# Kernel optimization log

Measured on AMD Instinct MI355X. Metric: run time of the kernel, lower is better.

## Reference

```python
import jax, jax.numpy as jnp
import numpy as np
from jax.ops import segment_sum, segment_max

N, E, F, H, G, P, C = 50000, 600000, 128, 128, 64, 32, 10
HEADS = 3
BN_EPS = 1e-5
COS_EPS = 1e-8


def setup_inputs() -> dict:
    key = jax.random.key(0)
    ks = jax.random.split(key, 32)
    rn = lambda k, shape, s: jax.random.normal(k, shape, jnp.float32) * s
    inp = {
        "x": jax.random.normal(ks[0], (N, F), jnp.float32),
        "edge_index": jax.random.randint(ks[1], (2, E), 0, N, jnp.int32),
        "batch": jnp.sort(jax.random.randint(ks[2], (N,), 0, G, jnp.int32)),
        # GCNConv
        "W1": rn(ks[3], (F, H), F ** -0.5), "b1": jnp.zeros((H,), jnp.float32),
        # SAGEConv (lin_l on aggregated neighbors, lin_r on root)
        "Wl": rn(ks[4], (H, H), H ** -0.5), "Wr": rn(ks[5], (H, H), H ** -0.5),
        "bs": jnp.zeros((H,), jnp.float32),
        # GATConv, heads=3, concat=False
        "Wg": rn(ks[6], (H, HEADS * H), H ** -0.5),
        "a_src": rn(ks[7], (HEADS, H), H ** -0.5),
        "a_dst": rn(ks[8], (HEADS, H), H ** -0.5),
        "bg": jnp.zeros((H,), jnp.float32),
        # prototype head / classifier / decoder
        "protos": jax.random.normal(ks[9], (P, H), jnp.float32),
        "Wc": rn(ks[10], (H, C), H ** -0.5), "bc": jnp.zeros((C,), jnp.float32),
        "Wd1": rn(ks[11], (H, 2 * H), H ** -0.5), "bd1": jnp.zeros((2 * H,), jnp.float32),
        "Wd2": rn(ks[12], (2 * H, F), (2 * H) ** -0.5), "bd2": jnp.zeros((F,), jnp.float32),
    }
    # BatchNorm (eval mode): gamma, beta, running mean/var for bn1..bn3
    for i in range(3):
        k0, k1, k2 = jax.random.split(ks[13 + i], 3)
        inp[f"g{i+1}"] = 1.0 + rn(k0, (H,), 0.05)
        inp[f"be{i+1}"] = rn(k1, (H,), 0.05)
        inp[f"m{i+1}"] = rn(k2, (H,), 0.1)
        inp[f"v{i+1}"] = jnp.ones((H,), jnp.float32)
    return inp


def _bn(x, g, b, m, v):
    return (x - m) * jax.lax.rsqrt(v + BN_EPS) * g + b


def _forward(x, edge_index, batch,
             W1, b1, g1, be1, m1, v1,
             Wl, Wr, bs, g2, be2, m2, v2,
             Wg, a_src, a_dst, bg, g3, be3, m3, v3,
             protos, Wc, bc, Wd1, bd1, Wd2, bd2):
    src, dst = edge_index[0], edge_index[1]
    ones_e = jnp.ones((src.shape[0],), x.dtype)

    # --- GCNConv: symmetric norm with self-loops ---
    h = x @ W1                                        # [N, H]
    deg = segment_sum(ones_e, dst, num_segments=N) + 1.0
    dinv = jax.lax.rsqrt(deg)
    coef = dinv[src] * dinv[dst]                      # [E]
    h1 = segment_sum(h[src] * coef[:, None], dst, num_segments=N)
    h1 = h1 + h * (dinv * dinv)[:, None] + b1         # self-loop term + bias
    h1 = jax.nn.elu(_bn(h1, g1, be1, m1, v1))         # dropout = identity (eval)

    # --- SAGEConv: mean aggregation (no self-loops) ---
    cnt = segment_sum(ones_e, dst, num_segments=N)
    mean_nb = segment_sum(h1[src], dst, num_segments=N) / jnp.maximum(cnt, 1.0)[:, None]
    h2 = mean_nb @ Wl + h1 @ Wr + bs
    h2 = jax.nn.elu(_bn(h2, g2, be2, m2, v2))

    # --- GATConv: heads=3, concat=False (mean), with self-loops ---
    hg = (h2 @ Wg).reshape(N, HEADS, H)               # [N, 3, H]
    al_src = jnp.einsum('nhf,hf->nh', hg, a_src)      # [N, 3]
    al_dst = jnp.einsum('nhf,hf->nh', hg, a_dst)
    loop = jnp.arange(N, dtype=src.dtype)
    s2 = jnp.concatenate([src, loop])
    d2 = jnp.concatenate([dst, loop])
    e = jax.nn.leaky_relu(al_src[s2] + al_dst[d2], 0.2)   # [E+N, 3]
    emax = segment_max(e, d2, num_segments=N)             # every node has a self-loop
    ex = jnp.exp(e - emax[d2])
    den = segment_sum(ex, d2, num_segments=N)
    alpha = ex / den[d2]                                  # [E+N, 3]
    h3 = segment_sum(hg[s2] * alpha[:, :, None], d2, num_segments=N)
    h3 = h3.mean(axis=1) + bg                             # concat=False -> head mean
    h3 = jax.nn.elu(_bn(h3, g3, be3, m3, v3))

    # --- global mean pool over graphs ---
    gcnt = segment_sum(jnp.ones((N,), x.dtype), batch, num_segments=G)
    pooled = segment_sum(h3, batch, num_segments=G) / jnp.maximum(gcnt, 1.0)[:, None]

    # --- prototype head: cosine sim -> softmax -> mix ---
    xn = pooled / jnp.maximum(jnp.linalg.norm(pooled, axis=-1, keepdims=True), COS_EPS)
    pn = protos / jnp.maximum(jnp.linalg.norm(protos, axis=-1, keepdims=True), COS_EPS)
    sims = xn @ pn.T                                      # [G, P]
    assignments = jax.nn.softmax(sims, axis=-1)
    proto_emb = assignments @ protos                      # [G, H]
    logits = proto_emb @ Wc + bc                          # [G, C]
    reconstructed = jax.nn.relu(pooled @ Wd1 + bd1) @ Wd2 + bd2   # [G, F]
    return logits, proto_emb, assignments, reconstructed


def reference(x, edge_index, batch,
              W1, b1, g1, be1, m1, v1,
              Wl, Wr, bs, g2, be2, m2, v2,
              Wg, a_src, a_dst, bg, g3, be3, m3, v3,
              protos, Wc, bc, Wd1, bd1, Wd2, bd2):
    return _forward(x, edge_index, batch,
                    W1, b1, g1, be1, m1, v1,
                    Wl, Wr, bs, g2, be2, m2, v2,
                    Wg, a_src, a_dst, bg, g3, be3, m3, v3,
                    protos, Wc, bc, Wd1, bd1, Wd2, bd2)
```

## Files before the change

kernel.cpp:

```cpp
#include <hip/hip_runtime.h>
#include <hip/hip_bf16.h>
#include <stdint.h>
#include <stddef.h>

#define N_ 50000
#define E_ 600000
#define F_ 128
#define H_ 128
#define G_ 64
#define P_ 32
#define C_ 10
#define NB_ 49

typedef __hip_bfloat16 bf16;
typedef __attribute__((ext_vector_type(8))) short short8;
typedef __attribute__((ext_vector_type(4))) float float4v;

__device__ __forceinline__ float b2f(bf16 x){ return __bfloat162float(x); }
__device__ __forceinline__ float us2f(unsigned short u){ return __uint_as_float(((unsigned int)u)<<16); }
__device__ __forceinline__ unsigned short f2us(float x){ bf16 h = __float2bfloat16(x); return *(unsigned short*)&h; }
__device__ __forceinline__ float eluf(float x){ return x>0.f ? x : expm1f(x); }
__device__ __forceinline__ float bnf(float x,float m,float v,float g,float b){ return (x-m)*rsqrtf(v+1e-5f)*g+b; }
__device__ __forceinline__ float lrelu(float x){ return x>0.f ? x : 0.2f*x; }
__device__ __forceinline__ float expc(float x){ return __expf(fminf(x, 50.f)); }
__device__ __forceinline__ void atomAddF(float* a, float v){ unsafeAtomicAdd(a, v); }

__global__ __launch_bounds__(256) void k_wprep(const float* __restrict__ W1, const float* __restrict__ Wl,
    const float* __restrict__ Wr, const float* __restrict__ Wg, unsigned short* __restrict__ WT){
  int idx = blockIdx.x*256 + threadIdx.x;
  if(idx >= 6*16384) return;
  int m = idx >> 14, rem = idx & 16383;
  int n = rem >> 7, k = rem & 127;
  float v;
  if(m==0)      v = W1[k*128+n];
  else if(m==1) v = Wl[k*128+n];
  else if(m==2) v = Wr[k*128+n];
  else          v = Wg[k*384 + (m-3)*128 + n];
  WT[idx] = f2us(v);
}

__device__ __forceinline__ void stage_WT(const unsigned short* __restrict__ WTg, unsigned short* lds, int tid){
  #pragma unroll
  for(int i=0;i<8;i++){
    int idx = tid + i*256;
    int n = idx>>4, c = idx&15;
    uint4 v = *(const uint4*)(WTg + (size_t)idx*8);
    int cs = c ^ (n & 15);
    *(uint4*)(lds + n*128 + cs*8) = v;
  }
}
__device__ __forceinline__ short8 read_Bfrag(const unsigned short* lds, int tile, int kc, int lane){
  int n = tile*16 + (lane&15);
  int c = kc*4 + (lane>>4);
  int cs = c ^ (lane & 15);
  return *(const short8*)(lds + n*128 + cs*8);
}
__device__ __forceinline__ void load_Afrag_bf16(const bf16* A, int row, int lane, short8 af[4]){
  const unsigned short* ap = (const unsigned short*)A + (size_t)row*128 + (lane>>4)*8;
  #pragma unroll
  for(int kc=0;kc<4;kc++) af[kc] = *(const short8*)(ap + kc*32);
}
__device__ __forceinline__ void mfma_pass(const unsigned short* lds, const short8 af[4], int lane, float4v acc[8]){
  #pragma unroll
  for(int tile=0;tile<8;tile++){
    #pragma unroll
    for(int kc=0;kc<4;kc++){
      short8 bfv = read_Bfrag(lds, tile, kc, lane);
      acc[tile] = __builtin_amdgcn_mfma_f32_16x16x32_bf16(af[kc], bfv, acc[tile], 0, 0, 0);
    }
  }
}

__global__ __launch_bounds__(256) void k_mm_x(const float* __restrict__ X, const unsigned short* __restrict__ WTg,
                                              bf16* __restrict__ HB){
  __shared__ unsigned short Wlds[128*128];
  const int tid = threadIdx.x, lane = tid&63, w = tid>>6;
  const int row0 = blockIdx.x*64;
  stage_WT(WTg, Wlds, tid);
  int arow = row0 + w*16 + (lane&15);
  int ar = arow < N_ ? arow : N_-1;
  const float* ap = X + (size_t)ar*128 + (lane>>4)*8;
  short8 af[4];
  #pragma unroll
  for(int kc=0;kc<4;kc++){
    float4 a = *(const float4*)(ap + kc*32);
    float4 b = *(const float4*)(ap + kc*32 + 4);
    short8 v;
    v[0]=(short)f2us(a.x); v[1]=(short)f2us(a.y); v[2]=(short)f2us(a.z); v[3]=(short)f2us(a.w);
    v[4]=(short)f2us(b.x); v[5]=(short)f2us(b.y); v[6]=(short)f2us(b.z); v[7]=(short)f2us(b.w);
    af[kc]=v;
  }
  __syncthreads();
  float4v acc[8];
  #pragma unroll
  for(int t=0;t<8;t++){ acc[t][0]=0.f; acc[t][1]=0.f; acc[t][2]=0.f; acc[t][3]=0.f; }
  mfma_pass(Wlds, af, lane, acc);
  const int colb = lane&15, q = lane>>4;
  unsigned short* ob = (unsigned short*)HB;
  #pragma unroll
  for(int r=0;r<4;r++){
    int ro = row0 + w*16 + q*4 + r;
    if(ro < N_){
      #pragma unroll
      for(int tile=0;tile<8;tile++)
        ob[(size_t)ro*128 + tile*16 + colb] = f2us(acc[tile][r]);
    }
  }
}

__global__ __launch_bounds__(256) void k_sage_mm(const bf16* __restrict__ MaB, const bf16* __restrict__ H1B,
    const unsigned short* __restrict__ WlT, const unsigned short* __restrict__ WrT,
    const float* __restrict__ bs, const float* __restrict__ g2, const float* __restrict__ be2,
    const float* __restrict__ m2, const float* __restrict__ v2, bf16* __restrict__ H2B){
  __shared__ unsigned short Wlds[128*128];
  const int tid = threadIdx.x, lane = tid&63, w = tid>>6;
  const int row0 = blockIdx.x*64;
  int arow = row0 + w*16 + (lane&15);
  int ar = arow < N_ ? arow : N_-1;
  float4v acc[8];
  #pragma unroll
  for(int t=0;t<8;t++){ acc[t][0]=0.f; acc[t][1]=0.f; acc[t][2]=0.f; acc[t][3]=0.f; }
  short8 af[4];

  stage_WT(WlT, Wlds, tid);
  load_Afrag_bf16(MaB, ar, lane, af);
  __syncthreads();
  mfma_pass(Wlds, af, lane, acc);
  __syncthreads();
  stage_WT(WrT, Wlds, tid);
  load_Afrag_bf16(H1B, ar, lane, af);
  __syncthreads();
  mfma_pass(Wlds, af, lane, acc);

  const int colb = lane&15, q = lane>>4;
  unsigned short* ob = (unsigned short*)H2B;
  #pragma unroll
  for(int tile=0;tile<8;tile++){
    int col = tile*16 + colb;
    float bsv=bs[col], gv=g2[col], bev=be2[col], mv=m2[col], vv=v2[col];
    #pragma unroll
    for(int r=0;r<4;r++){
      int ro = row0 + w*16 + q*4 + r;
      if(ro < N_){
        float x = acc[tile][r] + bsv;
        ob[(size_t)ro*128 + col] = f2us(eluf(bnf(x, mv, vv, gv, bev)));
      }
    }
  }
}

__global__ __launch_bounds__(256) void k_gat_mm(const bf16* __restrict__ H2B, const unsigned short* __restrict__ WgT,
    const float* __restrict__ a_src, const float* __restrict__ a_dst, int hh,
    bf16* __restrict__ HGH, float* __restrict__ als, float* __restrict__ ald){
  __shared__ unsigned short Wlds[128*128];
  const int tid = threadIdx.x, lane = tid&63, w = tid>>6;
  const int row0 = blockIdx.x*64;
  stage_WT(WgT, Wlds, tid);
  int arow = row0 + w*16 + (lane&15);
  int ar = arow < N_ ? arow : N_-1;
  short8 af[4];
  load_Afrag_bf16(H2B, ar, lane, af);
  __syncthreads();
  float4v acc[8];
  #pragma unroll
  for(int t=0;t<8;t++){ acc[t][0]=0.f; acc[t][1]=0.f; acc[t][2]=0.f; acc[t][3]=0.f; }
  mfma_pass(Wlds, af, lane, acc);

  const int colb = lane&15, q = lane>>4;
  float asv[8], adv[8];
  #pragma unroll
  for(int tile=0;tile<8;tile++){
    asv[tile] = a_src[hh*128 + tile*16 + colb];
    adv[tile] = a_dst[hh*128 + tile*16 + colb];
  }
  unsigned short* ob = (unsigned short*)HGH;
  #pragma unroll
  for(int r=0;r<4;r++){
    int ro = row0 + w*16 + q*4 + r;
    float ps = 0.f, pd = 0.f;
    #pragma unroll
    for(int tile=0;tile<8;tile++){ ps += acc[tile][r]*asv[tile]; pd += acc[tile][r]*adv[tile]; }
    #pragma unroll
    for(int o=8;o>0;o>>=1){ ps += __shfl_down(ps,o,16); pd += __shfl_down(pd,o,16); }
    if(ro < N_){
      #pragma unroll
      for(int tile=0;tile<8;tile++)
        ob[(size_t)ro*128 + tile*16 + colb] = f2us(acc[tile][r]);
      if(colb == 0){ als[ro] = ps; ald[ro] = pd; }
    }
  }
}

__global__ __launch_bounds__(256) void k_count(const int* __restrict__ dst, int* __restrict__ cnt){
  int e = blockIdx.x*256 + threadIdx.x;
  if(e < E_) atomicAdd(&cnt[dst[e]], 1);
}

__global__ __launch_bounds__(1024) void k_scan1(const int* __restrict__ cnt, int* __restrict__ row_ptr,
                                                float* __restrict__ dinv, int* __restrict__ bsum){
  __shared__ int wsum[16];
  const int t = threadIdx.x, lane = t & 63, wid = t >> 6;
  int i = blockIdx.x*1024 + t;
  int v = (i<N_) ? cnt[i] : 0;
  int x = v;
  #pragma unroll
  for(int o=1;o<64;o<<=1){
    int y = __shfl_up(x, o, 64);
    if(lane >= o) x += y;
  }
  if(lane==63) wsum[wid] = x;
  __syncthreads();
  if(wid==0){
    int s = (lane<16) ? wsum[lane] : 0;
    #pragma unroll
    for(int o=1;o<16;o<<=1){
      int y = __shfl_up(s, o, 64);
      if(lane >= o) s += y;
    }
    if(lane<16) wsum[lane] = s;
  }
  __syncthreads();
  int waveoff = (wid>0) ? wsum[wid-1] : 0;
  int incl = waveoff + x;
  if(i<N_){
    row_ptr[i] = incl - v;
    dinv[i] = rsqrtf((float)v + 1.f);
  }
  if(t==1023) bsum[blockIdx.x] = incl;
}

__global__ __launch_bounds__(64) void k_scan2(const int* __restrict__ bsum, int* __restrict__ boff,
                                              int* __restrict__ row_ptr){
  int lane = threadIdx.x;
  int v = (lane < NB_) ? bsum[lane] : 0;
  int x = v;
  #pragma unroll
  for(int o=1;o<64;o<<=1){
    int y = __shfl_up(x, o, 64);
    if(lane >= o) x += y;
  }
  if(lane < NB_) boff[lane] = x - v;
  if(lane == 63) row_ptr[N_] = x;
}

__global__ __launch_bounds__(256) void k_scan3(int* __restrict__ row_ptr, const int* __restrict__ boff,
                                               int* __restrict__ tmp){
  int i = blockIdx.x*256 + threadIdx.x;
  if(i < N_){
    int r = row_ptr[i] + boff[i>>10];
    row_ptr[i] = r;
    tmp[i] = r;
  }
}

__global__ __launch_bounds__(256) void k_scatter(const int* __restrict__ src, const int* __restrict__ dst,
                                                 int* __restrict__ tmp, int* __restrict__ esrc){
  int e = blockIdx.x*256 + threadIdx.x;
  if(e < E_){
    int d = dst[e];
    int pos = atomicAdd(&tmp[d], 1);
    esrc[pos] = src[e];
  }
}

__global__ __launch_bounds__(256) void k_gcn_gather(const int* __restrict__ row_ptr, const int* __restrict__ esrc,
    const float* __restrict__ dinv, const bf16* __restrict__ HB,
    const float* __restrict__ b1, const float* __restrict__ g1, const float* __restrict__ be1,
    const float* __restrict__ m1, const float* __restrict__ v1, bf16* __restrict__ H1B){
  int n = blockIdx.x*4 + (threadIdx.x>>6);
  int lane = threadIdx.x & 63;
  if(n >= N_) return;
  int beg = row_ptr[n], end = row_ptr[n+1];
  float dn = dinv[n];
  float a0 = 0.f, a1 = 0.f;
  const unsigned short* hb = (const unsigned short*)HB;
  int e = beg;
  for(; e+3 < end; e += 4){
    int s0 = esrc[e], s1 = esrc[e+1], s2 = esrc[e+2], s3 = esrc[e+3];
    unsigned int hv0 = *(const unsigned int*)(hb + (size_t)s0*H_ + lane*2);
    unsigned int hv1 = *(const unsigned int*)(hb + (size_t)s1*H_ + lane*2);
    unsigned int hv2 = *(const unsigned int*)(hb + (size_t)s2*H_ + lane*2);
    unsigned int hv3 = *(const unsigned int*)(hb + (size_t)s3*H_ + lane*2);
    float c0 = dinv[s0]*dn, c1 = dinv[s1]*dn, c2 = dinv[s2]*dn, c3 = dinv[s3]*dn;
    a0 += c0*us2f((unsigned short)(hv0 & 0xFFFFu)) + c1*us2f((unsigned short)(hv1 & 0xFFFFu))
        + c2*us2f((unsigned short)(hv2 & 0xFFFFu)) + c3*us2f((unsigned short)(hv3 & 0xFFFFu));
    a1 += c0*us2f((unsigned short)(hv0 >> 16)) + c1*us2f((unsigned short)(hv1 >> 16))
        + c2*us2f((unsigned short)(hv2 >> 16)) + c3*us2f((unsigned short)(hv3 >> 16));
  }
  for(; e < end; e++){
    int s = esrc[e];
    float c = dinv[s]*dn;
    unsigned int hv = *(const unsigned int*)(hb + (size_t)s*H_ + lane*2);
    a0 += c*us2f((unsigned short)(hv & 0xFFFFu));
    a1 += c*us2f((unsigned short)(hv >> 16));
  }
  unsigned int hv = *(const unsigned int*)(hb + (size_t)n*H_ + lane*2);
  int f0 = lane*2, f1 = f0+1;
  float x0 = a0 + us2f((unsigned short)(hv & 0xFFFFu))*dn*dn + b1[f0];
  float x1 = a1 + us2f((unsigned short)(hv >> 16))*dn*dn + b1[f1];
  x0 = eluf(bnf(x0, m1[f0], v1[f0], g1[f0], be1[f0]));
  x1 = eluf(bnf(x1, m1[f1], v1[f1], g1[f1], be1[f1]));
  unsigned int o = ((unsigned int)f2us(x1)<<16) | f2us(x0);
  *(unsigned int*)((unsigned short*)H1B + (size_t)n*H_ + lane*2) = o;
}

__global__ __launch_bounds__(256) void k_sage_gather(const int* __restrict__ row_ptr, const int* __restrict__ esrc,
    const bf16* __restrict__ H1B, bf16* __restrict__ MeanB){
  int n = blockIdx.x*4 + (threadIdx.x>>6);
  int lane = threadIdx.x & 63;
  if(n >= N_) return;
  int beg = row_ptr[n], end = row_ptr[n+1];
  float a0 = 0.f, a1 = 0.f;
  const unsigned short* hb = (const unsigned short*)H1B;
  int e = beg;
  for(; e+3 < end; e += 4){
    int s0 = esrc[e], s1 = esrc[e+1], s2 = esrc[e+2], s3 = esrc[e+3];
    unsigned int hv0 = *(const unsigned int*)(hb + (size_t)s0*H_ + lane*2);
    unsigned int hv1 = *(const unsigned int*)(hb + (size_t)s1*H_ + lane*2);
    unsigned int hv2 = *(const unsigned int*)(hb + (size_t)s2*H_ + lane*2);
    unsigned int hv3 = *(const unsigned int*)(hb + (size_t)s3*H_ + lane*2);
    a0 += us2f((unsigned short)(hv0 & 0xFFFFu)) + us2f((unsigned short)(hv1 & 0xFFFFu))
        + us2f((unsigned short)(hv2 & 0xFFFFu)) + us2f((unsigned short)(hv3 & 0xFFFFu));
    a1 += us2f((unsigned short)(hv0 >> 16)) + us2f((unsigned short)(hv1 >> 16))
        + us2f((unsigned short)(hv2 >> 16)) + us2f((unsigned short)(hv3 >> 16));
  }
  for(; e < end; e++){
    unsigned int hv = *(const unsigned int*)(hb + (size_t)esrc[e]*H_ + lane*2);
    a0 += us2f((unsigned short)(hv & 0xFFFFu));
    a1 += us2f((unsigned short)(hv >> 16));
  }
  float inv = 1.f / fmaxf((float)(end-beg), 1.f);
  unsigned int o = ((unsigned int)f2us(a1*inv)<<16) | f2us(a0*inv);
  *(unsigned int*)((unsigned short*)MeanB + (size_t)n*H_ + lane*2) = o;
}

__global__ __launch_bounds__(256) void k_gat_gather(const int* __restrict__ row_ptr, const int* __restrict__ esrc,
    const float* __restrict__ als, const float* __restrict__ ald, const bf16* __restrict__ HGH,
    int hh, bf16* __restrict__ ACCB){
  int n = blockIdx.x*4 + (threadIdx.x>>6);
  int lane = threadIdx.x & 63;
  if(n >= N_) return;
  int beg = row_ptr[n], end = row_ptr[n+1];
  float aldn = ald[n];
  float eself = expc(lrelu(als[n] + aldn));
  const unsigned short* hb = (const unsigned short*)HGH;
  unsigned int hv = *(const unsigned int*)(hb + (size_t)n*H_ + lane*2);
  float den = eself;
  float a0 = eself*us2f((unsigned short)(hv & 0xFFFFu));
  float a1 = eself*us2f((unsigned short)(hv >> 16));
  int e = beg;
  for(; e+3 < end; e += 4){
    int s0 = esrc[e], s1 = esrc[e+1], s2 = esrc[e+2], s3 = esrc[e+3];
    unsigned int sv0 = *(const unsigned int*)(hb + (size_t)s0*H_ + lane*2);
    unsigned int sv1 = *(const unsigned int*)(hb + (size_t)s1*H_ + lane*2);
    unsigned int sv2 = *(const unsigned int*)(hb + (size_t)s2*H_ + lane*2);
    unsigned int sv3 = *(const unsigned int*)(hb + (size_t)s3*H_ + lane*2);
    float w0 = expc(lrelu(als[s0] + aldn));
    float w1 = expc(lrelu(als[s1] + aldn));
    float w2 = expc(lrelu(als[s2] + aldn));
    float w3 = expc(lrelu(als[s3] + aldn));
    den += w0 + w1 + w2 + w3;
    a0 += w0*us2f((unsigned short)(sv0 & 0xFFFFu)) + w1*us2f((unsigned short)(sv1 & 0xFFFFu))
        + w2*us2f((unsigned short)(sv2 & 0xFFFFu)) + w3*us2f((unsigned short)(sv3 & 0xFFFFu));
    a1 += w0*us2f((unsigned short)(sv0 >> 16)) + w1*us2f((unsigned short)(sv1 >> 16))
        + w2*us2f((unsigned short)(sv2 >> 16)) + w3*us2f((unsigned short)(sv3 >> 16));
  }
  for(; e < end; e++){
    int s = esrc[e];
    float w = expc(lrelu(als[s] + aldn));
    unsigned int sv = *(const unsigned int*)(hb + (size_t)s*H_ + lane*2);
    den += w;
    a0 += w*us2f((unsigned short)(sv & 0xFFFFu));
    a1 += w*us2f((unsigned short)(sv >> 16));
  }
  float inv = 1.f/(3.f*den);
  a0 *= inv; a1 *= inv;
  unsigned int* acc = (unsigned int*)((unsigned short*)ACCB + (size_t)n*H_ + lane*2);
  if(hh != 0){
    unsigned int old = *acc;
    a0 += us2f((unsigned short)(old & 0xFFFFu));
    a1 += us2f((unsigned short)(old >> 16));
  }
  *acc = ((unsigned int)f2us(a1)<<16) | f2us(a0);
}

#define NPW_ 16
__global__ __launch_bounds__(256) void k_h3fin_pool(const bf16* __restrict__ ACCB, const float* __restrict__ bg,
    const float* __restrict__ g3, const float* __restrict__ be3, const float* __restrict__ m3, const float* __restrict__ v3,
    const int* __restrict__ batch, float* __restrict__ pooled, float* __restrict__ gcnt){
  int wave = blockIdx.x*4 + (threadIdx.x>>6);
  int lane = threadIdx.x & 63;
  int n0 = wave*NPW_;
  if(n0 >= N_) return;
  int n1 = n0 + NPW_; if(n1 > N_) n1 = N_;
  int f0 = lane*2, f1 = f0+1;
  float bg0=bg[f0], bg1=bg[f1];
  float g30=g3[f0], g31=g3[f1], be30=be3[f0], be31=be3[f1];
  float m30=m3[f0], m31=m3[f1], v30=v3[f0], v31=v3[f1];
  float r0=0.f, r1=0.f;
  int cur = batch[n0];
  int seg = 0;
  for(int n=n0; n<n1; n++){
    int b = batch[n];
    if(b != cur){
      atomAddF(&pooled[cur*H_ + f0], r0);
      atomAddF(&pooled[cur*H_ + f1], r1);
      if(lane==0) atomAddF(&gcnt[cur], (float)seg);
      r0 = 0.f; r1 = 0.f; seg = 0; cur = b;
    }
    unsigned int hv = *(const unsigned int*)((const unsigned short*)ACCB + (size_t)n*H_ + lane*2);
    float x0 = us2f((unsigned short)(hv & 0xFFFFu)) + bg0;
    float x1 = us2f((unsigned short)(hv >> 16)) + bg1;
    r0 += eluf(bnf(x0, m30, v30, g30, be30));
    r1 += eluf(bnf(x1, m31, v31, g31, be31));
    seg++;
  }
  atomAddF(&pooled[cur*H_ + f0], r0);
  atomAddF(&pooled[cur*H_ + f1], r1);
  if(lane==0) atomAddF(&gcnt[cur], (float)seg);
}

__global__ __launch_bounds__(128) void k_head(const float* __restrict__ pooledacc, const float* __restrict__ gcnt,
    const float* __restrict__ protos, const float* __restrict__ Wc, const float* __restrict__ bc,
    const float* __restrict__ Wd1, const float* __restrict__ bd1, const float* __restrict__ Wd2, const float* __restrict__ bd2,
    float* __restrict__ out){
  const int g = blockIdx.x, t = threadIdx.x;
  __shared__ float p[128], xn[128], red[128], sims[32], es[32], asg[32], pe[128], t1[256];
  __shared__ float nrm;
  float cg_ = fmaxf(gcnt[g], 1.f);
  p[t] = pooledacc[g*128 + t] / cg_;
  __syncthreads();
  red[t] = p[t]*p[t];
  __syncthreads();
  for(int s=64;s>0;s>>=1){ if(t<s) red[t]+=red[t+s]; __syncthreads(); }
  if(t==0) nrm = fmaxf(sqrtf(red[0]), 1e-8f);
  __syncthreads();
  xn[t] = p[t]/nrm;
  __syncthreads();
  if(t<32){
    float s=0.f, pn=0.f;
    for(int f=0;f<128;f++){ float pv=protos[t*128+f]; s += xn[f]*pv; pn += pv*pv; }
    sims[t] = s / fmaxf(sqrtf(pn), 1e-8f);
  }
  __syncthreads();
  if(t<32){
    float mx=-1e30f;
    for(int j=0;j<32;j++) mx = fmaxf(mx, sims[j]);
    es[t] = __expf(sims[t]-mx);
  }
  __syncthreads();
  if(t<32){
    float sm=0.f;
    for(int j=0;j<32;j++) sm += es[j];
    float a = es[t]/fmaxf(sm,1e-20f);
    asg[t] = a;
    out[8832 + g*32 + t] = a;
  }
  __syncthreads();
  {
    float s=0.f;
    for(int pp=0;pp<32;pp++) s += asg[pp]*protos[pp*128+t];
    pe[t] = s;
    out[640 + g*128 + t] = s;
  }
  __syncthreads();
  if(t<10){
    float s = bc[t];
    for(int f=0;f<128;f++) s += pe[f]*Wc[f*10+t];
    out[g*10 + t] = s;
  }
  for(int j=t;j<256;j+=128){
    float s = bd1[j];
    for(int f=0;f<128;f++) s += p[f]*Wd1[f*256+j];
    t1[j] = fmaxf(s, 0.f);
  }
  __syncthreads();
  {
    float s = bd2[t];
    for(int j=0;j<256;j++) s += t1[j]*Wd2[j*128+t];
    out[10880 + g*128 + t] = s;
  }
}

__global__ void k_sentinel(float* out, float code){
  out[0] = code;
}

extern "C" void kernel_launch(void* const* d_in, const int* in_sizes, int n_in,
                              void* d_out, int out_size, void* d_ws, size_t ws_size,
                              hipStream_t stream){
  const float* X    = (const float*)d_in[0];
  const int*  EI    = (const int*)d_in[1];
  const int*  batch = (const int*)d_in[2];
  const int* src = EI;
  const int* dst = EI + E_;

  int iW1,ib1,iWl,iWr,ibs,iWg,ias,iad,ibg,ipr,iWc,ibc,iWd1,ibd1,iWd2,ibd2;
  int ig1,ibe1,im1,iv1,ig2,ibe2,im2,iv2,ig3,ibe3,im3,iv3;
  if(n_in >= 31 && in_sizes[5] == 128){
    iW1=3; ib1=4; ig1=5; ibe1=6; im1=7; iv1=8;
    iWl=9; iWr=10; ibs=11; ig2=12; ibe2=13; im2=14; iv2=15;
    iWg=16; ias=17; iad=18; ibg=19; ig3=20; ibe3=21; im3=22; iv3=23;
    ipr=24; iWc=25; ibc=26; iWd1=27; ibd1=28; iWd2=29; ibd2=30;
  }else{
    iW1=3; ib1=4; iWl=5; iWr=6; ibs=7; iWg=8; ias=9; iad=10; ibg=11;
    ipr=12; iWc=13; ibc=14; iWd1=15; ibd1=16; iWd2=17; ibd2=18;
    ig1=19; ibe1=20; im1=21; iv1=22; ig2=23; ibe2=24; im2=25; iv2=26;
    ig3=27; ibe3=28; im3=29; iv3=30;
  }
  const float* W1 = (const float*)d_in[iW1];   const float* b1 = (const float*)d_in[ib1];
  const float* Wl = (const float*)d_in[iWl];   const float* Wr = (const float*)d_in[iWr];
  const float* bs = (const float*)d_in[ibs];   const float* Wg = (const float*)d_in[iWg];
  const float* a_src = (const float*)d_in[ias]; const float* a_dst = (const float*)d_in[iad];
  const float* bg = (const float*)d_in[ibg];   const float* protos = (const float*)d_in[ipr];
  const float* Wc = (const float*)d_in[iWc];   const float* bc = (const float*)d_in[ibc];
  const float* Wd1 = (const float*)d_in[iWd1]; const float* bd1 = (const float*)d_in[ibd1];
  const float* Wd2 = (const float*)d_in[iWd2]; const float* bd2 = (const float*)d_in[ibd2];
  const float* g1 = (const float*)d_in[ig1];   const float* be1 = (const float*)d_in[ibe1];
  const float* m1 = (const float*)d_in[im1];   const float* v1 = (const float*)d_in[iv1];
  const float* g2 = (const float*)d_in[ig2];   const float* be2 = (const float*)d_in[ibe2];
  const float* m2 = (const float*)d_in[im2];   const float* v2 = (const float*)d_in[iv2];
  const float* g3 = (const float*)d_in[ig3];   const float* be3 = (const float*)d_in[ibe3];
  const float* m3 = (const float*)d_in[im3];   const float* v3 = (const float*)d_in[iv3];

  const size_t NF = (size_t)N_*H_;
  const size_t intN = (size_t)N_ + (N_+1) + N_ + E_ + 128;
  const size_t fltN = (size_t)3*N_ + G_*H_ + G_;
  const size_t NEED = NF*2*3 + intN*4 + fltN*4 + (size_t)6*16384*2;
  if(ws_size < NEED){
    k_sentinel<<<1,1,0,stream>>>((float*)d_out, 1000.f + (float)(ws_size>>20));
    return;
  }
  bf16* RA = (bf16*)d_ws;
  bf16* RB = RA + NF;
  bf16* RC = RB + NF;
  int*  cnt     = (int*)(RC + NF);
  int*  row_ptr = cnt + N_;
  int*  tmp     = row_ptr + (N_+1);
  int*  esrc    = tmp + N_;
  int*  bsum    = esrc + E_;
  int*  boff    = bsum + 64;
  float* dinv   = (float*)(boff + 64);
  float* als    = dinv + N_;
  float* ald    = als + N_;
  float* pooled = ald + N_;
  float* gcnt   = pooled + (size_t)G_*H_;
  unsigned short* WTg = (unsigned short*)(gcnt + G_);

  k_wprep<<<(6*16384+255)/256, 256, 0, stream>>>(W1, Wl, Wr, Wg, WTg);
  hipMemsetAsync(cnt, 0, N_*sizeof(int), stream);
  k_count<<<(E_+255)/256, 256, 0, stream>>>(dst, cnt);
  k_scan1<<<NB_, 1024, 0, stream>>>(cnt, row_ptr, dinv, bsum);
  k_scan2<<<1, 64, 0, stream>>>(bsum, boff, row_ptr);
  k_scan3<<<(N_+255)/256, 256, 0, stream>>>(row_ptr, boff, tmp);
  k_scatter<<<(E_+255)/256, 256, 0, stream>>>(src, dst, tmp, esrc);

  const int GB = (N_+3)/4;
  const int MB = (N_+63)/64;
  k_mm_x<<<MB, 256, 0, stream>>>(X, WTg, RA);
  k_gcn_gather<<<GB, 256, 0, stream>>>(row_ptr, esrc, dinv, RA, b1, g1, be1, m1, v1, RB);
  k_sage_gather<<<GB, 256, 0, stream>>>(row_ptr, esrc, RB, RC);
  k_sage_mm<<<MB, 256, 0, stream>>>(RC, RB, WTg + 16384, WTg + 2*16384, bs, g2, be2, m2, v2, RA);
  for(int hh=0; hh<3; hh++){
    k_gat_mm<<<MB, 256, 0, stream>>>(RA, WTg + (3+hh)*16384, a_src, a_dst, hh, RB, als, ald);
    k_gat_gather<<<GB, 256, 0, stream>>>(row_ptr, esrc, als, ald, RB, hh, RC);
  }
  hipMemsetAsync(pooled, 0, (size_t)(G_*H_+G_)*sizeof(float), stream);
  {
    int waves = (N_ + NPW_ - 1)/NPW_;
    int blocks = (waves + 3)/4;
    k_h3fin_pool<<<blocks, 256, 0, stream>>>(RC, bg, g3, be3, m3, v3, batch, pooled, gcnt);
  }
  k_head<<<G_, 128, 0, stream>>>(pooled, gcnt, protos, Wc, bc, Wd1, bd1, Wd2, bd2, (float*)d_out);
}
```

Before: 482.3 us.

## Fuse three GAT heads into one matmul and one gather kernel

Replaces the per-head loop of GAT matmul plus gather launches with a single matmul kernel that computes all three heads into an interleaved [N,384] buffer, and a single gather that walks each edge list once for all heads. This removes four kernel launches, reads of the edge lists and row pointers three times, and the read-modify-write of the bf16 accumulator between heads, which also drops the intermediate bf16 rounding. In exchange it needs a larger workspace, and the gather now issues three row loads per edge with more registers and only 2-way unrolling.

```diff
diff --git a/kernel.cpp b/kernel.cpp
--- a/kernel.cpp
+++ b/kernel.cpp
@@ -149,44 +149,46 @@
   }
 }
 
-__global__ __launch_bounds__(256) void k_gat_mm(const bf16* __restrict__ H2B, const unsigned short* __restrict__ WgT,
-    const float* __restrict__ a_src, const float* __restrict__ a_dst, int hh,
-    bf16* __restrict__ HGH, float* __restrict__ als, float* __restrict__ ald){
+__global__ __launch_bounds__(256) void k_gat_mm_all(const bf16* __restrict__ H2B, const unsigned short* __restrict__ WgT,
+    const float* __restrict__ a_src, const float* __restrict__ a_dst,
+    bf16* __restrict__ HG3, float* __restrict__ als3, float* __restrict__ ald3){
   __shared__ unsigned short Wlds[128*128];
   const int tid = threadIdx.x, lane = tid&63, w = tid>>6;
   const int row0 = blockIdx.x*64;
-  stage_WT(WgT, Wlds, tid);
   int arow = row0 + w*16 + (lane&15);
   int ar = arow < N_ ? arow : N_-1;
   short8 af[4];
   load_Afrag_bf16(H2B, ar, lane, af);
-  __syncthreads();
-  float4v acc[8];
-  #pragma unroll
-  for(int t=0;t<8;t++){ acc[t][0]=0.f; acc[t][1]=0.f; acc[t][2]=0.f; acc[t][3]=0.f; }
-  mfma_pass(Wlds, af, lane, acc);
-
   const int colb = lane&15, q = lane>>4;
-  float asv[8], adv[8];
-  #pragma unroll
-  for(int tile=0;tile<8;tile++){
-    asv[tile] = a_src[hh*128 + tile*16 + colb];
-    adv[tile] = a_dst[hh*128 + tile*16 + colb];
-  }
-  unsigned short* ob = (unsigned short*)HGH;
-  #pragma unroll
-  for(int r=0;r<4;r++){
-    int ro = row0 + w*16 + q*4 + r;
-    float ps = 0.f, pd = 0.f;
+  unsigned short* ob = (unsigned short*)HG3;
+  for(int hh=0; hh<3; hh++){
+    if(hh) __syncthreads();
+    stage_WT(WgT + hh*16384, Wlds, tid);
+    __syncthreads();
+    float4v acc[8];
     #pragma unroll
-    for(int tile=0;tile<8;tile++){ ps += acc[tile][r]*asv[tile]; pd += acc[tile][r]*adv[tile]; }
+    for(int t=0;t<8;t++){ acc[t][0]=0.f; acc[t][1]=0.f; acc[t][2]=0.f; acc[t][3]=0.f; }
+    mfma_pass(Wlds, af, lane, acc);
+    float asv[8], adv[8];
     #pragma unroll
-    for(int o=8;o>0;o>>=1){ ps += __shfl_down(ps,o,16); pd += __shfl_down(pd,o,16); }
-    if(ro < N_){
+    for(int tile=0;tile<8;tile++){
+      asv[tile] = a_src[hh*128 + tile*16 + colb];
+      adv[tile] = a_dst[hh*128 + tile*16 + colb];
+    }
+    #pragma unroll
+    for(int r=0;r<4;r++){
+      int ro = row0 + w*16 + q*4 + r;
+      float ps = 0.f, pd = 0.f;
       #pragma unroll
-      for(int tile=0;tile<8;tile++)
-        ob[(size_t)ro*128 + tile*16 + colb] = f2us(acc[tile][r]);
-      if(colb == 0){ als[ro] = ps; ald[ro] = pd; }
+      for(int tile=0;tile<8;tile++){ ps += acc[tile][r]*asv[tile]; pd += acc[tile][r]*adv[tile]; }
+      #pragma unroll
+      for(int o=8;o>0;o>>=1){ ps += __shfl_down(ps,o,16); pd += __shfl_down(pd,o,16); }
+      if(ro < N_){
+        #pragma unroll
+        for(int tile=0;tile<8;tile++)
+          ob[(size_t)ro*384 + hh*128 + tile*16 + colb] = f2us(acc[tile][r]);
+        if(colb == 0){ als3[ro*3+hh] = ps; ald3[ro*3+hh] = pd; }
+      }
     }
   }
 }
@@ -334,54 +336,69 @@
   *(unsigned int*)((unsigned short*)MeanB + (size_t)n*H_ + lane*2) = o;
 }
 
-__global__ __launch_bounds__(256) void k_gat_gather(const int* __restrict__ row_ptr, const int* __restrict__ esrc,
-    const float* __restrict__ als, const float* __restrict__ ald, const bf16* __restrict__ HGH,
-    int hh, bf16* __restrict__ ACCB){
+__global__ __launch_bounds__(256) void k_gat_gather3(const int* __restrict__ row_ptr, const int* __restrict__ esrc,
+    const float* __restrict__ als3, const float* __restrict__ ald3, const bf16* __restrict__ HG3,
+    bf16* __restrict__ H3B){
   int n = blockIdx.x*4 + (threadIdx.x>>6);
   int lane = threadIdx.x & 63;
   if(n >= N_) return;
   int beg = row_ptr[n], end = row_ptr[n+1];
-  float aldn = ald[n];
-  float eself = expc(lrelu(als[n] + aldn));
-  const unsigned short* hb = (const unsigned short*)HGH;
-  unsigned int hv = *(const unsigned int*)(hb + (size_t)n*H_ + lane*2);
-  float den = eself;
-  float a0 = eself*us2f((unsigned short)(hv & 0xFFFFu));
-  float a1 = eself*us2f((unsigned short)(hv >> 16));
+  float ald0 = ald3[n*3+0], ald1 = ald3[n*3+1], ald2 = ald3[n*3+2];
+  float es0 = expc(lrelu(als3[n*3+0] + ald0));
+  float es1 = expc(lrelu(als3[n*3+1] + ald1));
+  float es2 = expc(lrelu(als3[n*3+2] + ald2));
+  const unsigned short* hb = (const unsigned short*)HG3;
+  size_t nb = (size_t)n*384 + lane*2;
+  unsigned int h0 = *(const unsigned int*)(hb + nb);
+  unsigned int h1 = *(const unsigned int*)(hb + nb + 128);
+  unsigned int h2 = *(const unsigned int*)(hb + nb + 256);
+  float den0 = es0, den1 = es1, den2 = es2;
+  float a00 = es0*us2f((unsigned short)(h0 & 0xFFFFu)), a01 = es0*us2f((unsigned short)(h0 >> 16));
+  float a10 = es1*us2f((unsigned short)(h1 & 0xFFFFu)), a11 = es1*us2f((unsigned short)(h1 >> 16));
+  float a20 = es2*us2f((unsigned short)(h2 & 0xFFFFu)), a21 = es2*us2f((unsigned short)(h2 >> 16));
   int e = beg;
-  for(; e+3 < end; e += 4){
-    int s0 = esrc[e], s1 = esrc[e+1], s2 = esrc[e+2], s3 = esrc[e+3];
-    unsigned int sv0 = *(const unsigned int*)(hb + (size_t)s0*H_ + lane*2);
-    unsigned int sv1 = *(const unsigned int*)(hb + (size_t)s1*H_ + lane*2);
-    unsigned int sv2 = *(const unsigned int*)(hb + (size_t)s2*H_ + lane*2);
-    unsigned int sv3 = *(const unsigned int*)(hb + (size_t)s3*H_ + lane*2);
-    float w0 = expc(lrelu(als[s0] + aldn));
-    float w1 = expc(lrelu(als[s1] + aldn));
-    float w2 = expc(lrelu(als[s2] + aldn));
-    float w3 = expc(lrelu(als[s3] + aldn));
-    den += w0 + w1 + w2 + w3;
-    a0 += w0*us2f((unsigned short)(sv0 & 0xFFFFu)) + w1*us2f((unsigned short)(sv1 & 0xFFFFu))
-        + w2*us2f((unsigned short)(sv2 & 0xFFFFu)) + w3*us2f((unsigned short)(sv3 & 0xFFFFu));
-    a1 += w0*us2f((unsigned short)(sv0 >> 16)) + w1*us2f((unsigned short)(sv1 >> 16))
-        + w2*us2f((unsigned short)(sv2 >> 16)) + w3*us2f((unsigned short)(sv3 >> 16));
-  }
-  for(; e < end; e++){
+  for(; e+1 < end; e += 2){
+    int s0 = esrc[e], s1 = esrc[e+1];
+    size_t b0 = (size_t)s0*384 + lane*2, b1 = (size_t)s1*384 + lane*2;
+    unsigned int p00 = *(const unsigned int*)(hb + b0);
+    unsigned int p01 = *(const unsigned int*)(hb + b0 + 128);
+    unsigned int p02 = *(const unsigned int*)(hb + b0 + 256);
+    unsigned int p10 = *(const unsigned int*)(hb + b1);
+    unsigned int p11 = *(const unsigned int*)(hb + b1 + 128);
+    unsigned int p12 = *(const unsigned int*)(hb + b1 + 256);
+    float w00 = expc(lrelu(als3[s0*3+0] + ald0));
+    float w01 = expc(lrelu(als3[s0*3+1] + ald1));
+    float w02 = expc(lrelu(als3[s0*3+2] + ald2));
+    float w10 = expc(lrelu(als3[s1*3+0] + ald0));
+    float w11 = expc(lrelu(als3[s1*3+1] + ald1));
+    float w12 = expc(lrelu(als3[s1*3+2] + ald2));
+    den0 += w00 + w10; den1 += w01 + w11; den2 += w02 + w12;
+    a00 += w00*us2f((unsigned short)(p00 & 0xFFFFu)) + w10*us2f((unsigned short)(p10 & 0xFFFFu));
+    a01 += w00*us2f((unsigned short)(p00 >> 16))     + w10*us2f((unsigned short)(p10 >> 16));
+    a10 += w01*us2f((unsigned short)(p01 & 0xFFFFu)) + w11*us2f((unsigned short)(p11 & 0xFFFFu));
+    a11 += w01*us2f((unsigned short)(p01 >> 16))     + w11*us2f((unsigned short)(p11 >> 16));
+    a20 += w02*us2f((unsigned short)(p02 & 0xFFFFu)) + w12*us2f((unsigned short)(p12 & 0xFFFFu));
+    a21 += w02*us2f((unsigned short)(p02 >> 16))     + w12*us2f((unsigned short)(p12 >> 16));
+  }
+  if(e < end){
     int s = esrc[e];
-    float w = expc(lrelu(als[s] + aldn));
-    unsigned int sv = *(const unsigned int*)(hb + (size_t)s*H_ + lane*2);
-    den += w;
-    a0 += w*us2f((unsigned short)(sv & 0xFFFFu));
-    a1 += w*us2f((unsigned short)(sv >> 16));
-  }
-  float inv = 1.f/(3.f*den);
-  a0 *= inv; a1 *= inv;
-  unsigned int* acc = (unsigned int*)((unsigned short*)ACCB + (size_t)n*H_ + lane*2);
-  if(hh != 0){
-    unsigned int old = *acc;
-    a0 += us2f((unsigned short)(old & 0xFFFFu));
-    a1 += us2f((unsigned short)(old >> 16));
-  }
-  *acc = ((unsigned int)f2us(a1)<<16) | f2us(a0);
+    size_t b0 = (size_t)s*384 + lane*2;
+    unsigned int p0 = *(const unsigned int*)(hb + b0);
+    unsigned int p1 = *(const unsigned int*)(hb + b0 + 128);
+    unsigned int p2 = *(const unsigned int*)(hb + b0 + 256);
+    float w0 = expc(lrelu(als3[s*3+0] + ald0));
+    float w1 = expc(lrelu(als3[s*3+1] + ald1));
+    float w2 = expc(lrelu(als3[s*3+2] + ald2));
+    den0 += w0; den1 += w1; den2 += w2;
+    a00 += w0*us2f((unsigned short)(p0 & 0xFFFFu)); a01 += w0*us2f((unsigned short)(p0 >> 16));
+    a10 += w1*us2f((unsigned short)(p1 & 0xFFFFu)); a11 += w1*us2f((unsigned short)(p1 >> 16));
+    a20 += w2*us2f((unsigned short)(p2 & 0xFFFFu)); a21 += w2*us2f((unsigned short)(p2 >> 16));
+  }
+  float i0 = 1.f/(3.f*den0), i1 = 1.f/(3.f*den1), i2 = 1.f/(3.f*den2);
+  float r0 = a00*i0 + a10*i1 + a20*i2;
+  float r1 = a01*i0 + a11*i1 + a21*i2;
+  unsigned int o = ((unsigned int)f2us(r1)<<16) | f2us(r0);
+  *(unsigned int*)((unsigned short*)H3B + (size_t)n*H_ + lane*2) = o;
 }
 
 #define NPW_ 16
@@ -525,8 +542,8 @@
 
   const size_t NF = (size_t)N_*H_;
   const size_t intN = (size_t)N_ + (N_+1) + N_ + E_ + 128;
-  const size_t fltN = (size_t)3*N_ + G_*H_ + G_;
-  const size_t NEED = NF*2*3 + intN*4 + fltN*4 + (size_t)6*16384*2;
+  const size_t fltN = (size_t)6*N_ + G_*H_ + G_;
+  const size_t NEED = NF*2*3 + (size_t)N_*384*2 + intN*4 + fltN*4 + (size_t)6*16384*2;
   if(ws_size < NEED){
     k_sentinel<<<1,1,0,stream>>>((float*)d_out, 1000.f + (float)(ws_size>>20));
     return;
@@ -534,16 +551,17 @@
   bf16* RA = (bf16*)d_ws;
   bf16* RB = RA + NF;
   bf16* RC = RB + NF;
-  int*  cnt     = (int*)(RC + NF);
+  bf16* HG3 = RC + NF;
+  int*  cnt     = (int*)(HG3 + (size_t)N_*384);
   int*  row_ptr = cnt + N_;
   int*  tmp     = row_ptr + (N_+1);
   int*  esrc    = tmp + N_;
   int*  bsum    = esrc + E_;
   int*  boff    = bsum + 64;
   float* dinv   = (float*)(boff + 64);
-  float* als    = dinv + N_;
-  float* ald    = als + N_;
-  float* pooled = ald + N_;
+  float* als3   = dinv + N_;
+  float* ald3   = als3 + (size_t)N_*3;
+  float* pooled = ald3 + (size_t)N_*3;
   float* gcnt   = pooled + (size_t)G_*H_;
   unsigned short* WTg = (unsigned short*)(gcnt + G_);
 
@@ -561,10 +579,8 @@
   k_gcn_gather<<<GB, 256, 0, stream>>>(row_ptr, esrc, dinv, RA, b1, g1, be1, m1, v1, RB);
   k_sage_gather<<<GB, 256, 0, stream>>>(row_ptr, esrc, RB, RC);
   k_sage_mm<<<MB, 256, 0, stream>>>(RC, RB, WTg + 16384, WTg + 2*16384, bs, g2, be2, m2, v2, RA);
-  for(int hh=0; hh<3; hh++){
-    k_gat_mm<<<MB, 256, 0, stream>>>(RA, WTg + (3+hh)*16384, a_src, a_dst, hh, RB, als, ald);
-    k_gat_gather<<<GB, 256, 0, stream>>>(row_ptr, esrc, als, ald, RB, hh, RC);
-  }
+  k_gat_mm_all<<<MB, 256, 0, stream>>>(RA, WTg + 3*16384, a_src, a_dst, HG3, als3, ald3);
+  k_gat_gather3<<<GB, 256, 0, stream>>>(row_ptr, esrc, als3, ald3, HG3, RC);
   hipMemsetAsync(pooled, 0, (size_t)(G_*H_+G_)*sizeof(float), stream);
   {
     int waves = (N_ + NPW_ - 1)/NPW_;
```

New measurement: 435.2 us. -9.8%, faster.
